# Optimization experiments

Hardware: AMD Instinct MI355X
Metric: run time of the kernel (lower is better)

The kernel has to match this reference:

```python
import jax, jax.numpy as jnp
import numpy as np

B, T, IN, H = 4096, 128, 768, 256


def setup_inputs() -> dict:
    key = jax.random.key(0)
    ks = jax.random.split(key, 5)
    s1 = 1.0 / np.sqrt(IN)
    s2 = 1.0 / np.sqrt(H)
    return {
        "x": jax.random.normal(ks[0], (B, IN), jnp.float32),
        "W1": jax.random.normal(ks[1], (T, IN, H), jnp.float32) * s1,
        "b1": jnp.zeros((T, H), jnp.float32),
        "W2": jax.random.normal(ks[2], (T, H, H), jnp.float32) * s2,
        "b2": jnp.zeros((T, H), jnp.float32),
        "W3": jax.random.normal(ks[3], (T, H), jnp.float32) * s2,
        "b3": jnp.zeros((T,), jnp.float32),
    }


def reference(x, W1, b1, W2, b2, W3, b3):
    # Per-task 3-layer MLP, vectorized over tasks. Dropout is eval-mode (identity).
    h = jax.nn.relu(jnp.einsum('bi,tih->bth', x, W1) + b1)          # [B, T, H]
    h = jax.nn.relu(jnp.einsum('bth,thk->btk', h, W2) + b2)         # [B, T, H]
    out = jnp.einsum('bth,th->bt', h, W3) + b3                      # [B, T]
    return out
```

## Files before the change

### kernel.cpp

```cpp
#include <hip/hip_runtime.h>
#include <cstdint>
#include <cstddef>

#define B_   4096
#define T_   128
#define IN_  768
#define H_   256
#define BM_  256
#define KC1  (IN_ / 32)
#define KC2  (H_ / 32)

typedef __bf16 bf16_t;
typedef bf16_t bf16x8 __attribute__((ext_vector_type(8)));
typedef bf16_t bf16x4 __attribute__((ext_vector_type(4)));
typedef float  floatx16 __attribute__((ext_vector_type(16)));

#define MFMA32(a, b, c) __builtin_amdgcn_mfma_f32_32x32x16_bf16((a), (b), (c), 0, 0, 0)

__device__ __forceinline__ void gl_lds16(const bf16_t* g, bf16_t* l) {
    __builtin_amdgcn_global_load_lds(
        (const __attribute__((address_space(1))) void*)g,
        (__attribute__((address_space(3))) void*)l, 16, 0, 0);
}

__global__ __launch_bounds__(256)
void tile_w2(const float* __restrict__ src, bf16_t* __restrict__ dst, int K, int KC) {
    const int t  = blockIdx.x / KC;
    const int kc = blockIdx.x - t * KC;
    const int kq = threadIdx.x >> 6;
    const int h4 = (threadIdx.x & 63) * 4;
    const float* s = src + ((size_t)t * K + kc * 32 + kq * 8) * H_ + h4;
    float r[8][4];
#pragma unroll
    for (int e = 0; e < 8; ++e) {
        float4 v = *(const float4*)(s + (size_t)e * H_);
        r[e][0] = v.x; r[e][1] = v.y; r[e][2] = v.z; r[e][3] = v.w;
    }
    bf16_t* d = dst + (((size_t)(t * KC + kc) * 4 + kq) * H_ + h4) * 8;
#pragma unroll
    for (int c = 0; c < 4; ++c) {
        bf16x8 v;
#pragma unroll
        for (int e = 0; e < 8; ++e) v[e] = (bf16_t)r[e][c];
        *(bf16x8*)(d + c * 8) = v;
    }
}

__global__ void tile_x_kernel(const float* __restrict__ src, bf16_t* __restrict__ dst,
                              long long total8) {
    long long o = (long long)blockIdx.x * blockDim.x + threadIdx.x;
    if (o >= total8) return;
    int m = (int)(o & 127);
    long long q = o >> 7;
    int kq = (int)(q & 3);
    int q2 = (int)(q >> 2);
    int kc   = q2 % KC1;
    int mblk = q2 / KC1;
    const float* s = src + ((long long)mblk * 128 + m) * IN_ + kc * 32 + kq * 8;
    float4 a = *(const float4*)s;
    float4 b = *(const float4*)(s + 4);
    bf16x8 v;
    v[0] = (bf16_t)a.x; v[1] = (bf16_t)a.y; v[2] = (bf16_t)a.z; v[3] = (bf16_t)a.w;
    v[4] = (bf16_t)b.x; v[5] = (bf16_t)b.y; v[6] = (bf16_t)b.z; v[7] = (bf16_t)b.w;
    *(bf16x8*)(dst + o * 8) = v;
}

__global__ __launch_bounds__(512, 2)
void mtmlp_fused3(const bf16_t* __restrict__ xt, const bf16_t* __restrict__ w1t,
                  const float* __restrict__ b1, const bf16_t* __restrict__ w2t,
                  const float* __restrict__ b2, const float* __restrict__ W3,
                  const float* __restrict__ b3, float* __restrict__ out) {
    const int L    = blockIdx.x;
    const int xcd  = L & 7;
    const int slot = L >> 3;
    const int t    = xcd * 16 + (slot >> 4);
    const int mblk = slot & 15;
    const int m0   = mblk * BM_;
    const int mb0  = mblk * 2;

    const int tid  = threadIdx.x;
    const int lane = tid & 63;
    const int wid  = tid >> 6;
    const int wm   = wid >> 2;
    const int wn   = wid & 3;
    const int ln31 = lane & 31;
    const int hi   = lane >> 5;

    __shared__ __align__(16) bf16_t hbuf[BM_ * H_];
    __shared__ __align__(16) bf16_t wt2[4 * H_ * 8];
    float* w3s = (float*)wt2;

    floatx16 acc[4][2];
#pragma unroll
    for (int i = 0; i < 4; ++i)
#pragma unroll
        for (int j = 0; j < 2; ++j)
#pragma unroll
            for (int e = 0; e < 16; ++e) acc[i][j][e] = 0.0f;

    const bf16_t* w1base = w1t + (size_t)t * KC1 * 8192;
    const bf16_t* x0base = xt + (size_t)mb0 * KC1 * 4096;
    const bf16_t* x1base = xt + (size_t)(mb0 + 1) * KC1 * 4096;

    auto stage1 = [&](bf16_t* buf, int kc) {
        const bf16_t* ws = w1base + (size_t)kc * 8192;
        gl_lds16(ws + tid * 8,        buf + tid * 8);
        gl_lds16(ws + 4096 + tid * 8, buf + 4096 + tid * 8);
        gl_lds16(x0base + (size_t)kc * 4096 + tid * 8, buf + 8192 + tid * 8);
        gl_lds16(x1base + (size_t)kc * 4096 + tid * 8, buf + 12288 + tid * 8);
    };
    auto comp1 = [&](const bf16_t* buf) {
#pragma unroll
        for (int s = 0; s < 2; ++s) {
            const int kq = s * 2 + hi;
            bf16x8 A[4], Bf[2];
#pragma unroll
            for (int i = 0; i < 4; ++i)
                A[i] = *(const bf16x8*)(buf + (size_t)(kq * H_ + wm * 128 + i * 32 + ln31) * 8);
#pragma unroll
            for (int j = 0; j < 2; ++j) {
                const int mm = wn * 64 + j * 32 + ln31;
                Bf[j] = *(const bf16x8*)(buf + 8192 + (mm >> 7) * 4096 +
                                         (size_t)(kq * 128 + (mm & 127)) * 8);
            }
#pragma unroll
            for (int i = 0; i < 4; ++i)
#pragma unroll
                for (int j = 0; j < 2; ++j) acc[i][j] = MFMA32(A[i], Bf[j], acc[i][j]);
        }
    };

    bf16_t* buf0 = hbuf;
    bf16_t* buf1 = hbuf + 16384;
    stage1(buf0, 0);
    for (int kc = 0; kc < KC1; kc += 2) {
        __syncthreads();
        stage1(buf1, kc + 1);
        comp1(buf0);
        __syncthreads();
        if (kc + 2 < KC1) stage1(buf0, kc + 2);
        comp1(buf1);
    }
    __syncthreads();

#pragma unroll
    for (int i = 0; i < 4; ++i) {
#pragma unroll
        for (int g = 0; g < 4; ++g) {
            const int h0 = wm * 128 + i * 32 + g * 8 + 4 * hi;
            float4 bias = *(const float4*)(b1 + t * H_ + h0);
            const int blk = h0 >> 3;
#pragma unroll
            for (int j = 0; j < 2; ++j) {
                const int mm = wn * 64 + j * 32 + ln31;
                bf16x4 o;
                o[0] = (bf16_t)fmaxf(acc[i][j][4 * g + 0] + bias.x, 0.0f);
                o[1] = (bf16_t)fmaxf(acc[i][j][4 * g + 1] + bias.y, 0.0f);
                o[2] = (bf16_t)fmaxf(acc[i][j][4 * g + 2] + bias.z, 0.0f);
                o[3] = (bf16_t)fmaxf(acc[i][j][4 * g + 3] + bias.w, 0.0f);
                *(bf16x4*)(hbuf + (size_t)(blk * BM_ + mm) * 8 + 4 * hi) = o;
            }
        }
    }

#pragma unroll
    for (int i = 0; i < 4; ++i)
#pragma unroll
        for (int j = 0; j < 2; ++j)
#pragma unroll
            for (int e = 0; e < 16; ++e) acc[i][j][e] = 0.0f;

    const bf16_t* w2base = w2t + (size_t)t * KC2 * 8192;
    for (int kc = 0; kc < KC2; ++kc) {
        __syncthreads();
        const bf16_t* ws = w2base + (size_t)kc * 8192;
        gl_lds16(ws + tid * 8,        wt2 + tid * 8);
        gl_lds16(ws + 4096 + tid * 8, wt2 + 4096 + tid * 8);
        __syncthreads();
#pragma unroll
        for (int s = 0; s < 2; ++s) {
            const int kq = s * 2 + hi;
            bf16x8 A[4], Bf[2];
#pragma unroll
            for (int i = 0; i < 4; ++i)
                A[i] = *(const bf16x8*)(wt2 + (size_t)(kq * H_ + wm * 128 + i * 32 + ln31) * 8);
            const int blk = kc * 4 + kq;
#pragma unroll
            for (int j = 0; j < 2; ++j) {
                const int mm = wn * 64 + j * 32 + ln31;
                Bf[j] = *(const bf16x8*)(hbuf + (size_t)(blk * BM_ + mm) * 8);
            }
#pragma unroll
            for (int i = 0; i < 4; ++i)
#pragma unroll
                for (int j = 0; j < 2; ++j) acc[i][j] = MFMA32(A[i], Bf[j], acc[i][j]);
        }
    }

    __syncthreads();
    if (tid < H_) w3s[tid] = W3[t * H_ + tid];
#pragma unroll
    for (int i = 0; i < 4; ++i) {
#pragma unroll
        for (int g = 0; g < 4; ++g) {
            const int h0 = wm * 128 + i * 32 + g * 8 + 4 * hi;
            float4 bias = *(const float4*)(b2 + t * H_ + h0);
            const int blk = h0 >> 3;
#pragma unroll
            for (int j = 0; j < 2; ++j) {
                const int mm = wn * 64 + j * 32 + ln31;
                bf16x4 o;
                o[0] = (bf16_t)fmaxf(acc[i][j][4 * g + 0] + bias.x, 0.0f);
                o[1] = (bf16_t)fmaxf(acc[i][j][4 * g + 1] + bias.y, 0.0f);
                o[2] = (bf16_t)fmaxf(acc[i][j][4 * g + 2] + bias.z, 0.0f);
                o[3] = (bf16_t)fmaxf(acc[i][j][4 * g + 3] + bias.w, 0.0f);
                *(bf16x4*)(hbuf + (size_t)(blk * BM_ + mm) * 8 + 4 * hi) = o;
            }
        }
    }
    __syncthreads();

    {
        const int m = tid >> 1, seg = tid & 1;
        float sum = 0.0f;
#pragma unroll
        for (int b = 0; b < 16; ++b) {
            const int blk = seg * 16 + b;
            const bf16x8 v = *(const bf16x8*)(hbuf + (size_t)(blk * BM_ + m) * 8);
            const float* w = w3s + blk * 8;
#pragma unroll
            for (int e = 0; e < 8; ++e) sum += (float)v[e] * w[e];
        }
        sum += __shfl_xor(sum, 1);
        if (seg == 0) out[(size_t)(m0 + m) * T_ + t] = sum + b3[t];
    }
}

extern "C" void kernel_launch(void* const* d_in, const int* in_sizes, int n_in,
                              void* d_out, int out_size, void* d_ws, size_t ws_size,
                              hipStream_t stream) {
    const float* x  = (const float*)d_in[0];
    const float* W1 = (const float*)d_in[1];
    const float* b1 = (const float*)d_in[2];
    const float* W2 = (const float*)d_in[3];
    const float* b2 = (const float*)d_in[4];
    const float* W3 = (const float*)d_in[5];
    const float* b3 = (const float*)d_in[6];
    float* out = (float*)d_out;

    const size_t nx  = (size_t)B_ * IN_;
    const size_t nw1 = (size_t)T_ * IN_ * H_;
    const size_t nw2 = (size_t)T_ * H_ * H_;

    bf16_t* xt  = (bf16_t*)d_ws;
    bf16_t* w1t = xt + nx;
    bf16_t* w2t = w1t + nw1;

    tile_x_kernel<<<dim3((unsigned)(nx / 8 / 256)), 256, 0, stream>>>(x, xt, (long long)(nx / 8));
    tile_w2<<<dim3(T_ * KC1), 256, 0, stream>>>(W1, w1t, IN_, KC1);
    tile_w2<<<dim3(T_ * KC2), 256, 0, stream>>>(W2, w2t, H_, KC2);

    mtmlp_fused3<<<dim3(2048), 512, 0, stream>>>(xt, w1t, b1, w2t, b2, W3, b3, out);
}
```

Before: 475.3 us.

## Deepen layer-1 pipeline to four stages and prefetch W2 with manual waitcnt barriers

Replaces the two-buffer layer-1 K loop with a four-buffer ring that keeps three global-to-LDS stages in flight, synchronised by explicit s_waitcnt vmcnt plus s_barrier instead of __syncthreads. The first two W2 tiles are prefetched during the layer-1 tail, and layer 2 now double-buffers W2 in an enlarged LDS buffer so loads overlap MFMA work. The goal is to hide global load latency and cut full barrier drains. It costs extra LDS for the second W2 buffer and relies on hand-counted vmcnt values, which are easy to get wrong.

```diff
diff --git a/kernel.cpp b/kernel.cpp
--- a/kernel.cpp
+++ b/kernel.cpp
@@ -16,6 +16,10 @@
 typedef float  floatx16 __attribute__((ext_vector_type(16)));
 
 #define MFMA32(a, b, c) __builtin_amdgcn_mfma_f32_32x32x16_bf16((a), (b), (c), 0, 0, 0)
+
+#define WAITBAR(N) asm volatile("s_waitcnt vmcnt(" #N ") lgkmcnt(0)\n\ts_barrier" ::: "memory")
+#define BAR_ONLY() asm volatile("s_barrier" ::: "memory")
+#define WAIT_LGK_BAR() asm volatile("s_waitcnt lgkmcnt(0)\n\ts_barrier" ::: "memory")
 
 __device__ __forceinline__ void gl_lds16(const bf16_t* g, bf16_t* l) {
     __builtin_amdgcn_global_load_lds(
@@ -87,7 +91,7 @@
     const int hi   = lane >> 5;
 
     __shared__ __align__(16) bf16_t hbuf[BM_ * H_];
-    __shared__ __align__(16) bf16_t wt2[4 * H_ * 8];
+    __shared__ __align__(16) bf16_t wt2[2 * 4 * H_ * 8];
     float* w3s = (float*)wt2;
 
     floatx16 acc[4][2];
@@ -99,6 +103,7 @@
             for (int e = 0; e < 16; ++e) acc[i][j][e] = 0.0f;
 
     const bf16_t* w1base = w1t + (size_t)t * KC1 * 8192;
+    const bf16_t* w2base = w2t + (size_t)t * KC2 * 8192;
     const bf16_t* x0base = xt + (size_t)mb0 * KC1 * 4096;
     const bf16_t* x1base = xt + (size_t)(mb0 + 1) * KC1 * 4096;
 
@@ -109,6 +114,11 @@
         gl_lds16(x0base + (size_t)kc * 4096 + tid * 8, buf + 8192 + tid * 8);
         gl_lds16(x1base + (size_t)kc * 4096 + tid * 8, buf + 12288 + tid * 8);
     };
+    auto stage2 = [&](bf16_t* dstb, int kc) {
+        const bf16_t* ws = w2base + (size_t)kc * 8192;
+        gl_lds16(ws + tid * 8,        dstb + tid * 8);
+        gl_lds16(ws + 4096 + tid * 8, dstb + 4096 + tid * 8);
+    };
     auto comp1 = [&](const bf16_t* buf) {
 #pragma unroll
         for (int s = 0; s < 2; ++s) {
@@ -130,18 +140,25 @@
         }
     };
 
-    bf16_t* buf0 = hbuf;
-    bf16_t* buf1 = hbuf + 16384;
-    stage1(buf0, 0);
-    for (int kc = 0; kc < KC1; kc += 2) {
-        __syncthreads();
-        stage1(buf1, kc + 1);
-        comp1(buf0);
-        __syncthreads();
-        if (kc + 2 < KC1) stage1(buf0, kc + 2);
-        comp1(buf1);
-    }
-    __syncthreads();
+    stage1(hbuf,          0);
+    stage1(hbuf + 16384,  1);
+    stage1(hbuf + 32768,  2);
+
+    for (int kc4 = 0; kc4 < 5; ++kc4) {
+        const int kc = kc4 * 4;
+#pragma unroll
+        for (int j = 0; j < 4; ++j) {
+            WAITBAR(8);
+            stage1(hbuf + ((j + 3) & 3) * 16384, kc + j + 3);
+            comp1(hbuf + j * 16384);
+        }
+    }
+    WAITBAR(8); stage1(hbuf + 49152, 23); comp1(hbuf);
+    WAITBAR(8); stage2(wt2, 0);           comp1(hbuf + 16384);
+    WAITBAR(6); stage2(wt2 + 8192, 1);    comp1(hbuf + 32768);
+    WAITBAR(4);                           comp1(hbuf + 49152);
+
+    BAR_ONLY();
 
 #pragma unroll
     for (int i = 0; i < 4; ++i) {
@@ -170,20 +187,14 @@
 #pragma unroll
             for (int e = 0; e < 16; ++e) acc[i][j][e] = 0.0f;
 
-    const bf16_t* w2base = w2t + (size_t)t * KC2 * 8192;
-    for (int kc = 0; kc < KC2; ++kc) {
-        __syncthreads();
-        const bf16_t* ws = w2base + (size_t)kc * 8192;
-        gl_lds16(ws + tid * 8,        wt2 + tid * 8);
-        gl_lds16(ws + 4096 + tid * 8, wt2 + 4096 + tid * 8);
-        __syncthreads();
+    auto comp2 = [&](const bf16_t* wbuf, int kc) {
 #pragma unroll
         for (int s = 0; s < 2; ++s) {
             const int kq = s * 2 + hi;
             bf16x8 A[4], Bf[2];
 #pragma unroll
             for (int i = 0; i < 4; ++i)
-                A[i] = *(const bf16x8*)(wt2 + (size_t)(kq * H_ + wm * 128 + i * 32 + ln31) * 8);
+                A[i] = *(const bf16x8*)(wbuf + (size_t)(kq * H_ + wm * 128 + i * 32 + ln31) * 8);
             const int blk = kc * 4 + kq;
 #pragma unroll
             for (int j = 0; j < 2; ++j) {
@@ -195,9 +206,16 @@
 #pragma unroll
                 for (int j = 0; j < 2; ++j) acc[i][j] = MFMA32(A[i], Bf[j], acc[i][j]);
         }
-    }
-
-    __syncthreads();
+    };
+
+#pragma unroll
+    for (int kc = 0; kc < KC2; ++kc) {
+        if (kc < KC2 - 1) { WAITBAR(2); } else { WAITBAR(0); }
+        comp2(wt2 + (kc & 1) * 8192, kc);
+        BAR_ONLY();
+        if (kc < KC2 - 2) stage2(wt2 + (kc & 1) * 8192, kc + 2);
+    }
+
     if (tid < H_) w3s[tid] = W3[t * H_ + tid];
 #pragma unroll
     for (int i = 0; i < 4; ++i) {
@@ -218,7 +236,7 @@
             }
         }
     }
-    __syncthreads();
+    WAIT_LGK_BAR();
 
     {
         const int m = tid >> 1, seg = tid & 1;
```

New measurement: 451.7 us. 5.0% less time.

## Halve row tile, add multi-stage async pipeline, merge prep kernels

Applied to the files above, without the earlier changes.

Cuts the batch tile from 256 to 128 rows, with 256-thread blocks and 4096 workgroups, so LDS use per block shrinks and more blocks can be resident. Replaces __syncthreads with inline-asm s_waitcnt vmcnt/barrier pairs, so global-to-LDS loads stay in flight across compute. Layer 2 weight loads are prefetched during the tail of layer 1, then double-buffered in half-chunks. The three tiling/convert kernels are merged into a single launch. The per-tile W1/W2 reloads double because each weight tile now serves fewer rows, and the hand-written vmcnt counts carry a correctness risk.

```diff
diff --git a/kernel.cpp b/kernel.cpp
--- a/kernel.cpp
+++ b/kernel.cpp
@@ -6,7 +6,7 @@
 #define T_   128
 #define IN_  768
 #define H_   256
-#define BM_  256
+#define BM_  128
 #define KC1  (IN_ / 32)
 #define KC2  (H_ / 32)
 
@@ -17,16 +17,20 @@
 
 #define MFMA32(a, b, c) __builtin_amdgcn_mfma_f32_32x32x16_bf16((a), (b), (c), 0, 0, 0)
 
+#define WAITBAR(N) asm volatile("s_waitcnt vmcnt(" #N ") lgkmcnt(0)\n\ts_barrier" ::: "memory")
+#define WAIT_LGK_BAR() asm volatile("s_waitcnt lgkmcnt(0)\n\ts_barrier" ::: "memory")
+
 __device__ __forceinline__ void gl_lds16(const bf16_t* g, bf16_t* l) {
     __builtin_amdgcn_global_load_lds(
         (const __attribute__((address_space(1))) void*)g,
         (__attribute__((address_space(3))) void*)l, 16, 0, 0);
 }
 
-__global__ __launch_bounds__(256)
-void tile_w2(const float* __restrict__ src, bf16_t* __restrict__ dst, int K, int KC) {
-    const int t  = blockIdx.x / KC;
-    const int kc = blockIdx.x - t * KC;
+__device__ __forceinline__ void tile_w_body(const float* __restrict__ src,
+                                            bf16_t* __restrict__ dst,
+                                            int K, int KC, int blk) {
+    const int t  = blk / KC;
+    const int kc = blk - t * KC;
     const int kq = threadIdx.x >> 6;
     const int h4 = (threadIdx.x & 63) * 4;
     const float* s = src + ((size_t)t * K + kc * 32 + kq * 8) * H_ + h4;
@@ -46,10 +50,8 @@
     }
 }
 
-__global__ void tile_x_kernel(const float* __restrict__ src, bf16_t* __restrict__ dst,
-                              long long total8) {
-    long long o = (long long)blockIdx.x * blockDim.x + threadIdx.x;
-    if (o >= total8) return;
+__device__ __forceinline__ void tile_x_body(const float* __restrict__ src,
+                                            bf16_t* __restrict__ dst, long long o) {
     int m = (int)(o & 127);
     long long q = o >> 7;
     int kq = (int)(q & 3);
@@ -65,29 +67,43 @@
     *(bf16x8*)(dst + o * 8) = v;
 }
 
-__global__ __launch_bounds__(512, 2)
-void mtmlp_fused3(const bf16_t* __restrict__ xt, const bf16_t* __restrict__ w1t,
+__global__ __launch_bounds__(256)
+void prep_all(const float* __restrict__ x,  bf16_t* __restrict__ xt,
+              const float* __restrict__ W1, bf16_t* __restrict__ w1t,
+              const float* __restrict__ W2, bf16_t* __restrict__ w2t) {
+    const int b = blockIdx.x;
+    if (b < 1536) {
+        long long o = (long long)b * 256 + threadIdx.x;
+        tile_x_body(x, xt, o);
+    } else if (b < 1536 + 3072) {
+        tile_w_body(W1, w1t, IN_, KC1, b - 1536);
+    } else {
+        tile_w_body(W2, w2t, H_, KC2, b - 4608);
+    }
+}
+
+__global__ __launch_bounds__(256, 2)
+void mtmlp_fused4(const bf16_t* __restrict__ xt, const bf16_t* __restrict__ w1t,
                   const float* __restrict__ b1, const bf16_t* __restrict__ w2t,
                   const float* __restrict__ b2, const float* __restrict__ W3,
                   const float* __restrict__ b3, float* __restrict__ out) {
     const int L    = blockIdx.x;
     const int xcd  = L & 7;
     const int slot = L >> 3;
-    const int t    = xcd * 16 + (slot >> 4);
-    const int mblk = slot & 15;
+    const int t    = xcd * 16 + (slot >> 5);
+    const int mblk = slot & 31;
     const int m0   = mblk * BM_;
-    const int mb0  = mblk * 2;
 
     const int tid  = threadIdx.x;
     const int lane = tid & 63;
     const int wid  = tid >> 6;
-    const int wm   = wid >> 2;
-    const int wn   = wid & 3;
+    const int wm   = wid >> 1;
+    const int wn   = wid & 1;
     const int ln31 = lane & 31;
     const int hi   = lane >> 5;
 
     __shared__ __align__(16) bf16_t hbuf[BM_ * H_];
-    __shared__ __align__(16) bf16_t wt2[4 * H_ * 8];
+    __shared__ __align__(16) bf16_t wt2[2 * 2 * H_ * 8];
     float* w3s = (float*)wt2;
 
     floatx16 acc[4][2];
@@ -99,15 +115,23 @@
             for (int e = 0; e < 16; ++e) acc[i][j][e] = 0.0f;
 
     const bf16_t* w1base = w1t + (size_t)t * KC1 * 8192;
-    const bf16_t* x0base = xt + (size_t)mb0 * KC1 * 4096;
-    const bf16_t* x1base = xt + (size_t)(mb0 + 1) * KC1 * 4096;
+    const bf16_t* w2base = w2t + (size_t)t * KC2 * 8192;
+    const bf16_t* xbase  = xt + (size_t)mblk * KC1 * 4096;
 
     auto stage1 = [&](bf16_t* buf, int kc) {
         const bf16_t* ws = w1base + (size_t)kc * 8192;
         gl_lds16(ws + tid * 8,        buf + tid * 8);
+        gl_lds16(ws + 2048 + tid * 8, buf + 2048 + tid * 8);
         gl_lds16(ws + 4096 + tid * 8, buf + 4096 + tid * 8);
-        gl_lds16(x0base + (size_t)kc * 4096 + tid * 8, buf + 8192 + tid * 8);
-        gl_lds16(x1base + (size_t)kc * 4096 + tid * 8, buf + 12288 + tid * 8);
+        gl_lds16(ws + 6144 + tid * 8, buf + 6144 + tid * 8);
+        const bf16_t* xs = xbase + (size_t)kc * 4096;
+        gl_lds16(xs + tid * 8,        buf + 8192 + tid * 8);
+        gl_lds16(xs + 2048 + tid * 8, buf + 10240 + tid * 8);
+    };
+    auto stage2h = [&](bf16_t* dst, int n) {
+        const bf16_t* ws = w2base + (size_t)n * 4096;
+        gl_lds16(ws + tid * 8,        dst + tid * 8);
+        gl_lds16(ws + 2048 + tid * 8, dst + 2048 + tid * 8);
     };
     auto comp1 = [&](const bf16_t* buf) {
 #pragma unroll
@@ -120,8 +144,7 @@
 #pragma unroll
             for (int j = 0; j < 2; ++j) {
                 const int mm = wn * 64 + j * 32 + ln31;
-                Bf[j] = *(const bf16x8*)(buf + 8192 + (mm >> 7) * 4096 +
-                                         (size_t)(kq * 128 + (mm & 127)) * 8);
+                Bf[j] = *(const bf16x8*)(buf + 8192 + (size_t)(kq * 128 + mm) * 8);
             }
 #pragma unroll
             for (int i = 0; i < 4; ++i)
@@ -129,19 +152,33 @@
                 for (int j = 0; j < 2; ++j) acc[i][j] = MFMA32(A[i], Bf[j], acc[i][j]);
         }
     };
-
-    bf16_t* buf0 = hbuf;
-    bf16_t* buf1 = hbuf + 16384;
-    stage1(buf0, 0);
-    for (int kc = 0; kc < KC1; kc += 2) {
-        __syncthreads();
-        stage1(buf1, kc + 1);
-        comp1(buf0);
-        __syncthreads();
-        if (kc + 2 < KC1) stage1(buf0, kc + 2);
-        comp1(buf1);
-    }
-    __syncthreads();
+    auto comp2 = [&](const bf16_t* wbuf, int n) {
+        bf16x8 A[4], Bf[2];
+#pragma unroll
+        for (int i = 0; i < 4; ++i)
+            A[i] = *(const bf16x8*)(wbuf + (size_t)(hi * H_ + wm * 128 + i * 32 + ln31) * 8);
+        const int blk = n * 2 + hi;
+#pragma unroll
+        for (int j = 0; j < 2; ++j) {
+            const int mm = wn * 64 + j * 32 + ln31;
+            Bf[j] = *(const bf16x8*)(hbuf + (size_t)(blk * BM_ + mm) * 8);
+        }
+#pragma unroll
+        for (int i = 0; i < 4; ++i)
+#pragma unroll
+            for (int j = 0; j < 2; ++j) acc[i][j] = MFMA32(A[i], Bf[j], acc[i][j]);
+    };
+
+    bf16_t* s0 = hbuf;
+    bf16_t* s1 = hbuf + 12288;
+    stage1(s0, 0);
+    stage1(s1, 1);
+    for (int p = 0; p < 11; ++p) {
+        WAITBAR(6); comp1(s0); WAIT_LGK_BAR(); stage1(s0, 2 * p + 2);
+        WAITBAR(6); comp1(s1); WAIT_LGK_BAR(); stage1(s1, 2 * p + 3);
+    }
+    WAITBAR(6); comp1(s0); WAIT_LGK_BAR(); stage2h(wt2, 0); stage2h(wt2 + 4096, 1);
+    WAITBAR(4); comp1(s1); WAIT_LGK_BAR();
 
 #pragma unroll
     for (int i = 0; i < 4; ++i) {
@@ -170,35 +207,17 @@
 #pragma unroll
             for (int e = 0; e < 16; ++e) acc[i][j][e] = 0.0f;
 
-    const bf16_t* w2base = w2t + (size_t)t * KC2 * 8192;
-    for (int kc = 0; kc < KC2; ++kc) {
-        __syncthreads();
-        const bf16_t* ws = w2base + (size_t)kc * 8192;
-        gl_lds16(ws + tid * 8,        wt2 + tid * 8);
-        gl_lds16(ws + 4096 + tid * 8, wt2 + 4096 + tid * 8);
-        __syncthreads();
-#pragma unroll
-        for (int s = 0; s < 2; ++s) {
-            const int kq = s * 2 + hi;
-            bf16x8 A[4], Bf[2];
-#pragma unroll
-            for (int i = 0; i < 4; ++i)
-                A[i] = *(const bf16x8*)(wt2 + (size_t)(kq * H_ + wm * 128 + i * 32 + ln31) * 8);
-            const int blk = kc * 4 + kq;
-#pragma unroll
-            for (int j = 0; j < 2; ++j) {
-                const int mm = wn * 64 + j * 32 + ln31;
-                Bf[j] = *(const bf16x8*)(hbuf + (size_t)(blk * BM_ + mm) * 8);
-            }
-#pragma unroll
-            for (int i = 0; i < 4; ++i)
-#pragma unroll
-                for (int j = 0; j < 2; ++j) acc[i][j] = MFMA32(A[i], Bf[j], acc[i][j]);
-        }
-    }
-
-    __syncthreads();
-    if (tid < H_) w3s[tid] = W3[t * H_ + tid];
+    for (int np = 0; np < 8; ++np) {
+        const int n0 = 2 * np, n1 = 2 * np + 1;
+        WAITBAR(2);
+        comp2(wt2, n0); WAIT_LGK_BAR();
+        if (n0 < 14) stage2h(wt2, n0 + 2);
+        if (n1 < 15) { WAITBAR(2); } else { WAITBAR(0); }
+        comp2(wt2 + 4096, n1); WAIT_LGK_BAR();
+        if (n1 < 14) stage2h(wt2 + 4096, n1 + 2);
+    }
+
+    w3s[tid] = W3[t * H_ + tid];
 #pragma unroll
     for (int i = 0; i < 4; ++i) {
 #pragma unroll
@@ -218,7 +237,7 @@
             }
         }
     }
-    __syncthreads();
+    WAIT_LGK_BAR();
 
     {
         const int m = tid >> 1, seg = tid & 1;
@@ -250,15 +269,11 @@
 
     const size_t nx  = (size_t)B_ * IN_;
     const size_t nw1 = (size_t)T_ * IN_ * H_;
-    const size_t nw2 = (size_t)T_ * H_ * H_;
 
     bf16_t* xt  = (bf16_t*)d_ws;
     bf16_t* w1t = xt + nx;
     bf16_t* w2t = w1t + nw1;
 
-    tile_x_kernel<<<dim3((unsigned)(nx / 8 / 256)), 256, 0, stream>>>(x, xt, (long long)(nx / 8));
-    tile_w2<<<dim3(T_ * KC1), 256, 0, stream>>>(W1, w1t, IN_, KC1);
-    tile_w2<<<dim3(T_ * KC2), 256, 0, stream>>>(W2, w2t, H_, KC2);
-
-    mtmlp_fused3<<<dim3(2048), 512, 0, stream>>>(xt, w1t, b1, w2t, b2, W3, b3, out);
-}
+    prep_all<<<dim3(5632), 256, 0, stream>>>(x, xt, W1, w1t, W2, w2t);
+    mtmlp_fused4<<<dim3(4096), 256, 0, stream>>>(xt, w1t, b1, w2t, b2, W3, b3, out);
+}
```

New measurement: 479.5 us. No clear change (+0.9%).
